# Kernel optimization log

Measured on AMD Instinct MI355X. Metric: run time of the kernel, lower is better.

Reference implementation:

```python
import jax, jax.numpy as jnp
import numpy as np

N, C, LM, ELEMS = 1024, 128, 16, 10   # nodes, channels, lm components (lmax=3), elements
P1, P2, P3 = 4, 12, 30                # generalized-CG path counts per correlation order
DIMS = (1, 3)                         # output irreps kept: 0e (dim 1), 1o (dim 3)


def _sparse(rng, shape, density=0.15):
    # stand-in generalized Clebsch-Gordan U tensor: fixed, sparse constants
    a = rng.standard_normal(shape).astype(np.float32)
    return jnp.asarray(a * (rng.random(shape) < density))


def setup_inputs() -> dict:
    k = jax.random.split(jax.random.key(0), 2)
    rng = np.random.default_rng(0)
    inp = {
        'x': jax.random.normal(k[0], (N, C, LM), jnp.float32),
        'species': jax.random.randint(k[1], (N,), 0, ELEMS, jnp.int32),
    }
    for i, d in enumerate(DIMS):
        inp[f'U1_{i}'] = _sparse(rng, (d, LM, P1))
        inp[f'U2_{i}'] = _sparse(rng, (d, LM, LM, P2))
        inp[f'U3_{i}'] = _sparse(rng, (d, LM, LM, LM, P3))
        for nu, p in ((1, P1), (2, P2), (3, P3)):
            inp[f'W{nu}_{i}'] = jnp.asarray((rng.standard_normal((ELEMS, p, C)) / np.sqrt(p)).astype(np.float32))
        inp[f'Wlin_{i}'] = jnp.asarray(rng.standard_normal((C, C)).astype(np.float32))
    return inp


def _sym_contract(x, species, U1, U2, U3, W1, W2, W3):
    # MACE recursive symmetric contraction, highest correlation order first.
    # x: [n, c, m] (channels factored to separate axis); species selects per-element weights.
    out = jnp.einsum('Lijmp,npc,ncm->ncLij', U3, W3[species], x)          # nu = 3 term
    out = jnp.einsum('Lijp,npc->ncLij', U2, W2[species]) + out            # add nu = 2 basis
    out = jnp.einsum('ncLij,ncj->ncLi', out, x)                           # contract one power of x
    out = jnp.einsum('Lip,npc->ncLi', U1, W1[species]) + out              # add nu = 1 basis
    return jnp.einsum('ncLi,nci->ncL', out, x)                            # [n, c, dim_L]


def _forward(x, species, U1_0, U2_0, U3_0, W1_0, W2_0, W3_0, Wlin_0,
             U1_1, U2_1, U3_1, W1_1, W2_1, W3_1, Wlin_1):
    f0 = _sym_contract(x, species, U1_0, U2_0, U3_0, W1_0, W2_0, W3_0)    # [n, C, 1]
    f1 = _sym_contract(x, species, U1_1, U2_1, U3_1, W1_1, W2_1, W3_1)    # [n, C, 3]
    s = 1.0 / float(np.sqrt(C))                                            # e3nn.Linear path norm
    y0 = jnp.einsum('nc,ck->nk', f0[..., 0], Wlin_0) * s                  # 128x0e block
    y1 = jnp.einsum('nci,ck->nki', f1, Wlin_1) * s                        # 128x1o block
    return jnp.concatenate([y0, y1.reshape(y1.shape[0], -1)], axis=-1)    # [n, 128 + 384]


def reference(x, species, U1_0, U2_0, U3_0, W1_0, W2_0, W3_0, Wlin_0,
              U1_1, U2_1, U3_1, W1_1, W2_1, W3_1, Wlin_1):
    return _forward(x, species, U1_0, U2_0, U3_0, W1_0, W2_0, W3_0, Wlin_0,
                    U1_1, U2_1, U3_1, W1_1, W2_1, W3_1, Wlin_1)
```

## Files before the change

kernel.cpp:

```cpp
#include <hip/hip_runtime.h>
#include <hip/hip_fp16.h>

typedef float v2f __attribute__((ext_vector_type(2)));

#define NN    1024
#define CC    128
#define NELEM 10
#define NQ3   816
#define NQ2   136
#define NQ    968
#define KP    48
#define QT    11
#define NTILE 88

#define NL_OFF    0
#define CNT_OFF   40960
#define CALL_OFF  524288
#define F_OFF     20447232
#define UHAT_OFF  10485760

__device__ __constant__ int d_OFF2[16] = {0,16,31,45,58,70,81,91,100,108,115,121,126,130,133,135};
__device__ __constant__ int d_OFF3[16] = {0,136,256,361,452,530,596,651,696,732,760,781,796,806,812,815};

__global__ void k_usym(const float* __restrict__ U3_0, const float* __restrict__ U3_1,
                       const float* __restrict__ U2_0, const float* __restrict__ U2_1,
                       const float* __restrict__ U1_0, const float* __restrict__ U1_1,
                       float* __restrict__ uhat) {
    if (blockIdx.x < 64) {
        int tid = blockIdx.x * 256 + threadIdx.x;
        int Lout = tid >> 12;
        int r = tid & 4095;
        int a = r >> 8, b = (r >> 4) & 15, m = r & 15;
        if (a > b || b > m) return;
        int q = d_OFF3[a] + (d_OFF2[b] - d_OFF2[a]) + (m - b);
        const float* U = (Lout == 0) ? U3_0 : U3_1;
        int L = (Lout == 0) ? 0 : (Lout - 1);
        int P[6][3] = {{a,b,m},{a,m,b},{b,a,m},{b,m,a},{m,a,b},{m,b,a}};
        float s[30];
#pragma unroll
        for (int p = 0; p < 30; ++p) s[p] = 0.f;
        for (int t = 0; t < 6; ++t) {
            bool dup = false;
            for (int u = 0; u < t; ++u)
                if (P[u][0] == P[t][0] && P[u][1] == P[t][1] && P[u][2] == P[t][2]) dup = true;
            if (dup) continue;
            const float* src = U + ((((L * 16 + P[t][0]) * 16 + P[t][1]) * 16 + P[t][2]) * 30);
#pragma unroll
            for (int p = 0; p < 30; ++p) s[p] += src[p];
        }
        float* dst = uhat + ((size_t)Lout * NQ + q) * KP;
#pragma unroll
        for (int p = 0; p < 30; ++p) dst[p] = s[p];
#pragma unroll
        for (int p = 30; p < KP; ++p) dst[p] = 0.f;
    } else {
        int tid = (blockIdx.x - 64) * 256 + threadIdx.x;
        if (tid < 1024) {
            int Lout = tid >> 8;
            int r = tid & 255;
            int a = r >> 4, b = r & 15;
            if (a > b) return;
            int q = NQ3 + d_OFF2[a] + (b - a);
            const float* U = (Lout == 0) ? U2_0 : U2_1;
            int L = (Lout == 0) ? 0 : (Lout - 1);
            float* dst = uhat + ((size_t)Lout * NQ + q) * KP;
#pragma unroll
            for (int p = 0; p < 30; ++p) dst[p] = 0.f;
#pragma unroll
            for (int p = 0; p < 12; ++p) {
                float v = U[((L * 16 + a) * 16 + b) * 12 + p];
                if (a != b) v += U[((L * 16 + b) * 16 + a) * 12 + p];
                dst[30 + p] = v;
            }
#pragma unroll
            for (int p = 42; p < KP; ++p) dst[p] = 0.f;
        } else if (tid < 1024 + 64) {
            int s2 = tid - 1024;
            int Lout = s2 >> 4, i = s2 & 15;
            int q = NQ3 + NQ2 + i;
            const float* U = (Lout == 0) ? U1_0 : U1_1;
            int L = (Lout == 0) ? 0 : (Lout - 1);
            float* dst = uhat + ((size_t)Lout * NQ + q) * KP;
#pragma unroll
            for (int p = 0; p < 42; ++p) dst[p] = 0.f;
#pragma unroll
            for (int p = 0; p < 4; ++p) dst[42 + p] = U[(L * 16 + i) * 4 + p];
            dst[46] = 0.f; dst[47] = 0.f;
        }
    }
}

__global__ void k_plist(const int* __restrict__ species, int* __restrict__ nodelist,
                        int* __restrict__ counts) {
    __shared__ int cnt[NELEM];
    int t = threadIdx.x;
    if (t < NELEM) cnt[t] = 0;
    __syncthreads();
    int e = species[t];
    int pos = atomicAdd(&cnt[e], 1);
    nodelist[e * NN + pos] = t;
    __syncthreads();
    if (t < NELEM) counts[t] = cnt[t];
}

__global__ __launch_bounds__(256) void k_fold(
    const float* __restrict__ uhat,
    const float* __restrict__ W1_0, const float* __restrict__ W2_0, const float* __restrict__ W3_0,
    const float* __restrict__ W1_1, const float* __restrict__ W2_1, const float* __restrict__ W3_1,
    uint2* __restrict__ call4h) {
    __shared__ __align__(16) float uh_lds[4][QT][KP];
    int e  = blockIdx.x / NTILE;
    int qt = blockIdx.x % NTILE;
    int t = threadIdx.x;
    {
        const float4* src4 = (const float4*)uhat;
        float4* dst4 = (float4*)uh_lds;
        for (int i = t; i < 4 * QT * 12; i += 256) {
            int l = i / (QT * 12);
            int r = i - l * (QT * 12);
            int qloc = r / 12, p4 = r % 12;
            dst4[i] = src4[((size_t)l * NQ + qt * QT + qloc) * 12 + p4];
        }
    }
    int c  = t & 127;
    int qs = t >> 7;
    float wr[2][KP];
#pragma unroll
    for (int p = 0; p < 30; ++p) {
        wr[0][p] = W3_0[(e * 30 + p) * CC + c];
        wr[1][p] = W3_1[(e * 30 + p) * CC + c];
    }
#pragma unroll
    for (int p = 0; p < 12; ++p) {
        wr[0][30 + p] = W2_0[(e * 12 + p) * CC + c];
        wr[1][30 + p] = W2_1[(e * 12 + p) * CC + c];
    }
#pragma unroll
    for (int p = 0; p < 4; ++p) {
        wr[0][42 + p] = W1_0[(e * 4 + p) * CC + c];
        wr[1][42 + p] = W1_1[(e * 4 + p) * CC + c];
    }
    wr[0][46] = wr[0][47] = wr[1][46] = wr[1][47] = 0.f;
    __syncthreads();
    size_t base = ((size_t)e * CC + c) * NQ;
    for (int j = 0; j < 6; ++j) {
        int qloc = qs * 6 + j;
        if (qloc >= QT) break;
        int q = qt * QT + qloc;
        float r[4];
#pragma unroll
        for (int l = 0; l < 4; ++l) {
            const float4* up = (const float4*)uh_lds[l][qloc];
            const float* w = (l == 0) ? wr[0] : wr[1];
            float acc0 = 0.f, acc1 = 0.f, acc2 = 0.f, acc3 = 0.f;
#pragma unroll
            for (int p4 = 0; p4 < 12; ++p4) {
                float4 u = up[p4];
                acc0 = fmaf(u.x, w[p4 * 4 + 0], acc0);
                acc1 = fmaf(u.y, w[p4 * 4 + 1], acc1);
                acc2 = fmaf(u.z, w[p4 * 4 + 2], acc2);
                acc3 = fmaf(u.w, w[p4 * 4 + 3], acc3);
            }
            r[l] = (acc0 + acc1) + (acc2 + acc3);
        }
        __half2 h01 = __floats2half2_rn(r[0], r[1]);
        __half2 h23 = __floats2half2_rn(r[2], r[3]);
        uint2 v;
        v.x = *(unsigned int*)&h01;
        v.y = *(unsigned int*)&h23;
        call4h[base + q] = v;
    }
}

#define COEF(W0, W1, W2, W3) \
    uint2 pk = cf_lds[q]; \
    __half2 h01 = *(__half2*)&pk.x; __half2 h23 = *(__half2*)&pk.y; \
    float W0 = __half2float(h01.x), W1 = __half2float(h01.y); \
    float W2 = __half2float(h23.x), W3 = __half2float(h23.y);

#define CUBIC(A0, A1) { \
    _Pragma("unroll") for (int a = (A0); a < (A1); ++a) { \
        _Pragma("unroll") for (int b = a; b < 16; ++b) { \
            v2f pab = xv[a] * xv[b]; \
            _Pragma("unroll") for (int m = b; m < 16; ++m) { \
                COEF(wx, wy, wz, ww); v2f mo = pab * xv[m]; \
                a0 += mo * wx; a1 += mo * wy; a2 += mo * wz; a3 += mo * ww; ++q; } } } }

#define QUAD(A0, A1) { \
    _Pragma("unroll") for (int a = (A0); a < (A1); ++a) { \
        _Pragma("unroll") for (int b = a; b < 16; ++b) { \
            COEF(wx, wy, wz, ww); v2f mo = xv[a] * xv[b]; \
            a0 += mo * wx; a1 += mo * wy; a2 += mo * wz; a3 += mo * ww; ++q; } } }

__global__ __launch_bounds__(256) void k_eval(
    const float* __restrict__ x, const int* __restrict__ nodelist,
    const int* __restrict__ counts, const uint2* __restrict__ call4h,
    float4* __restrict__ fout) {
    __shared__ __align__(16) uint2 cf_lds[NQ];
    __shared__ __align__(16) v2f part[3][64][4];
    int ec = blockIdx.x;
    int e = ec >> 7;
    int c = ec & 127;
    int cnt = counts[e];
    const float4* cf4 = (const float4*)(call4h + (size_t)ec * NQ);
    int t = threadIdx.x;
    int slice = t >> 6;
    int lane  = t & 63;

    int i0 = lane * 2, i1 = i0 + 1;
    bool v0i = i0 < cnt, v1i = i1 < cnt;
    int n0 = v0i ? nodelist[e * NN + i0] : 0;
    int n1 = v1i ? nodelist[e * NN + i1] : 0;

    for (int i = t; i < NQ / 2; i += 256) ((float4*)cf_lds)[i] = cf4[i];

    for (int sb = 0; sb < cnt; sb += 128) {
        if (sb > 0) {
            i0 = sb + lane * 2; i1 = i0 + 1;
            v0i = i0 < cnt; v1i = i1 < cnt;
            n0 = v0i ? nodelist[e * NN + i0] : 0;
            n1 = v1i ? nodelist[e * NN + i1] : 0;
        }
        const float4* xp0 = (const float4*)(x + ((size_t)n0 * CC + c) * 16);
        const float4* xp1 = (const float4*)(x + ((size_t)n1 * CC + c) * 16);
        float4 p0 = xp0[0], p1 = xp0[1], p2 = xp0[2], p3 = xp0[3];
        float4 q0 = xp1[0], q1 = xp1[1], q2 = xp1[2], q3 = xp1[3];
        if (sb == 0) __syncthreads();
        v2f xv[16];
        xv[0]  = v2f{p0.x, q0.x}; xv[1]  = v2f{p0.y, q0.y};
        xv[2]  = v2f{p0.z, q0.z}; xv[3]  = v2f{p0.w, q0.w};
        xv[4]  = v2f{p1.x, q1.x}; xv[5]  = v2f{p1.y, q1.y};
        xv[6]  = v2f{p1.z, q1.z}; xv[7]  = v2f{p1.w, q1.w};
        xv[8]  = v2f{p2.x, q2.x}; xv[9]  = v2f{p2.y, q2.y};
        xv[10] = v2f{p2.z, q2.z}; xv[11] = v2f{p2.w, q2.w};
        xv[12] = v2f{p3.x, q3.x}; xv[13] = v2f{p3.y, q3.y};
        xv[14] = v2f{p3.z, q3.z}; xv[15] = v2f{p3.w, q3.w};
        if (!v0i) {
#pragma unroll
            for (int m = 0; m < 16; ++m) xv[m].x = 0.f;
        }
        if (!v1i) {
#pragma unroll
            for (int m = 0; m < 16; ++m) xv[m].y = 0.f;
        }
        v2f a0 = {0.f, 0.f}, a1 = {0.f, 0.f}, a2 = {0.f, 0.f}, a3 = {0.f, 0.f};
        int q;
        if (slice == 0) {
            q = 0;   CUBIC(0, 2);
        } else if (slice == 1) {
            q = 256; CUBIC(2, 4);
            q = NQ3; QUAD(0, 4);
        } else if (slice == 2) {
            q = 452; CUBIC(4, 7);
            q = NQ3 + 58; QUAD(4, 10);
        } else {
            q = 651; CUBIC(7, 16);
            q = NQ3 + 115; QUAD(10, 16);
            q = NQ3 + NQ2;
#pragma unroll
            for (int a = 0; a < 16; ++a) {
                COEF(wx, wy, wz, ww); v2f mo = xv[a];
                a0 += mo * wx; a1 += mo * wy; a2 += mo * wz; a3 += mo * ww; ++q;
            }
        }
        if (slice > 0) {
            part[slice - 1][lane][0] = a0; part[slice - 1][lane][1] = a1;
            part[slice - 1][lane][2] = a2; part[slice - 1][lane][3] = a3;
        }
        __syncthreads();
        if (slice == 0) {
            v2f s0 = a0 + part[0][lane][0] + part[1][lane][0] + part[2][lane][0];
            v2f s1 = a1 + part[0][lane][1] + part[1][lane][1] + part[2][lane][1];
            v2f s2 = a2 + part[0][lane][2] + part[1][lane][2] + part[2][lane][2];
            v2f s3 = a3 + part[0][lane][3] + part[1][lane][3] + part[2][lane][3];
            if (v0i) fout[(size_t)n0 * CC + c] = make_float4(s0.x, s1.x, s2.x, s3.x);
            if (v1i) fout[(size_t)n1 * CC + c] = make_float4(s0.y, s1.y, s2.y, s3.y);
        }
        __syncthreads();
    }
}

__global__ __launch_bounds__(256) void k_linear(
    const float4* __restrict__ fin, const float* __restrict__ Wlin0,
    const float* __restrict__ Wlin1, float* __restrict__ out) {
    __shared__ float4 fl[256];
    int t = threadIdx.x;
    fl[t] = fin[(size_t)blockIdx.x * 256 + t];
    __syncthreads();
    int nl = t >> 7, k = t & 127;
    int n = blockIdx.x * 2 + nl;
    float a0 = 0.f, a1 = 0.f, a2 = 0.f, a3 = 0.f;
#pragma unroll 8
    for (int c = 0; c < CC; ++c) {
        float4 f = fl[nl * CC + c];
        float w0 = Wlin0[c * CC + k];
        float w1 = Wlin1[c * CC + k];
        a0 = fmaf(f.x, w0, a0);
        a1 = fmaf(f.y, w1, a1);
        a2 = fmaf(f.z, w1, a2);
        a3 = fmaf(f.w, w1, a3);
    }
    const float s = 0.08838834764831845f;
    float* o = out + (size_t)n * 512;
    o[k] = a0 * s;
    o[128 + 3 * k + 0] = a1 * s;
    o[128 + 3 * k + 1] = a2 * s;
    o[128 + 3 * k + 2] = a3 * s;
}

extern "C" void kernel_launch(void* const* d_in, const int* in_sizes, int n_in,
                              void* d_out, int out_size, void* d_ws, size_t ws_size,
                              hipStream_t stream) {
    const float* x     = (const float*)d_in[0];
    const int*   spec  = (const int*)d_in[1];
    const float* U1_0  = (const float*)d_in[2];
    const float* U2_0  = (const float*)d_in[3];
    const float* U3_0  = (const float*)d_in[4];
    const float* W1_0  = (const float*)d_in[5];
    const float* W2_0  = (const float*)d_in[6];
    const float* W3_0  = (const float*)d_in[7];
    const float* Wl_0  = (const float*)d_in[8];
    const float* U1_1  = (const float*)d_in[9];
    const float* U2_1  = (const float*)d_in[10];
    const float* U3_1  = (const float*)d_in[11];
    const float* W1_1  = (const float*)d_in[12];
    const float* W2_1  = (const float*)d_in[13];
    const float* W3_1  = (const float*)d_in[14];
    const float* Wl_1  = (const float*)d_in[15];

    char* ws = (char*)d_ws;
    int*    nodelist = (int*)(ws + NL_OFF);
    int*    counts   = (int*)(ws + CNT_OFF);
    uint2*  call4h   = (uint2*)(ws + CALL_OFF);
    float*  uhat     = (float*)(ws + UHAT_OFF);
    float4* fbuf     = (float4*)(ws + F_OFF);

    k_usym<<<dim3(69), dim3(256), 0, stream>>>(U3_0, U3_1, U2_0, U2_1, U1_0, U1_1, uhat);
    k_plist<<<dim3(1), dim3(1024), 0, stream>>>(spec, nodelist, counts);
    k_fold<<<dim3(880), dim3(256), 0, stream>>>(uhat, W1_0, W2_0, W3_0,
                                                W1_1, W2_1, W3_1, call4h);
    k_eval<<<dim3(1280), dim3(256), 0, stream>>>(x, nodelist, counts, call4h, fbuf);
    k_linear<<<dim3(512), dim3(256), 0, stream>>>(fbuf, Wl_0, Wl_1, (float*)d_out);
}
```

Measured before the change: 75.13 us.

## Merge setup kernels, register-block eval over four nodes, widen linear

The species bucketing is folded into the U symmetrisation kernel, which removes one launch. The eval kernel now gives each block two channels. Each lane handles four nodes, so every coefficient LDS load feeds eight packed FMAs, and coefficients are converted from fp16 to fp32 once when staged into LDS. The linear kernel computes two nodes per thread so each Wlin load is reused. The cost is more registers per thread in eval and half as many blocks, which may hurt occupancy and load balance.

```diff
diff --git a/kernel.cpp b/kernel.cpp
--- a/kernel.cpp
+++ b/kernel.cpp
@@ -16,16 +16,18 @@
 #define NL_OFF    0
 #define CNT_OFF   40960
 #define CALL_OFF  524288
+#define UHAT_OFF  10485760
 #define F_OFF     20447232
-#define UHAT_OFF  10485760
 
 __device__ __constant__ int d_OFF2[16] = {0,16,31,45,58,70,81,91,100,108,115,121,126,130,133,135};
 __device__ __constant__ int d_OFF3[16] = {0,136,256,361,452,530,596,651,696,732,760,781,796,806,812,815};
 
-__global__ void k_usym(const float* __restrict__ U3_0, const float* __restrict__ U3_1,
-                       const float* __restrict__ U2_0, const float* __restrict__ U2_1,
-                       const float* __restrict__ U1_0, const float* __restrict__ U1_1,
-                       float* __restrict__ uhat) {
+__global__ void k_setup(const float* __restrict__ U3_0, const float* __restrict__ U3_1,
+                        const float* __restrict__ U2_0, const float* __restrict__ U2_1,
+                        const float* __restrict__ U1_0, const float* __restrict__ U1_1,
+                        const int* __restrict__ species,
+                        float* __restrict__ uhat, int* __restrict__ nodelist,
+                        int* __restrict__ counts) {
     if (blockIdx.x < 64) {
         int tid = blockIdx.x * 256 + threadIdx.x;
         int Lout = tid >> 12;
@@ -53,7 +55,7 @@
         for (int p = 0; p < 30; ++p) dst[p] = s[p];
 #pragma unroll
         for (int p = 30; p < KP; ++p) dst[p] = 0.f;
-    } else {
+    } else if (blockIdx.x < 69) {
         int tid = (blockIdx.x - 64) * 256 + threadIdx.x;
         if (tid < 1024) {
             int Lout = tid >> 8;
@@ -87,20 +89,21 @@
             for (int p = 0; p < 4; ++p) dst[42 + p] = U[(L * 16 + i) * 4 + p];
             dst[46] = 0.f; dst[47] = 0.f;
         }
-    }
-}
-
-__global__ void k_plist(const int* __restrict__ species, int* __restrict__ nodelist,
-                        int* __restrict__ counts) {
-    __shared__ int cnt[NELEM];
-    int t = threadIdx.x;
-    if (t < NELEM) cnt[t] = 0;
-    __syncthreads();
-    int e = species[t];
-    int pos = atomicAdd(&cnt[e], 1);
-    nodelist[e * NN + pos] = t;
-    __syncthreads();
-    if (t < NELEM) counts[t] = cnt[t];
+    } else {
+        __shared__ int cnt[NELEM];
+        int t = threadIdx.x;
+        if (t < NELEM) cnt[t] = 0;
+        __syncthreads();
+#pragma unroll
+        for (int j = 0; j < 4; ++j) {
+            int node = t * 4 + j;
+            int e = species[node];
+            int pos = atomicAdd(&cnt[e], 1);
+            nodelist[e * NN + pos] = node;
+        }
+        __syncthreads();
+        if (t < NELEM) counts[t] = cnt[t];
+    }
 }
 
 __global__ __launch_bounds__(256) void k_fold(
@@ -172,78 +175,104 @@
     }
 }
 
-#define COEF(W0, W1, W2, W3) \
-    uint2 pk = cf_lds[q]; \
-    __half2 h01 = *(__half2*)&pk.x; __half2 h23 = *(__half2*)&pk.y; \
-    float W0 = __half2float(h01.x), W1 = __half2float(h01.y); \
-    float W2 = __half2float(h23.x), W3 = __half2float(h23.y);
-
 #define CUBIC(A0, A1) { \
     _Pragma("unroll") for (int a = (A0); a < (A1); ++a) { \
         _Pragma("unroll") for (int b = a; b < 16; ++b) { \
-            v2f pab = xv[a] * xv[b]; \
+            v2f pabA = xvA[a] * xvA[b]; v2f pabB = xvB[a] * xvB[b]; \
             _Pragma("unroll") for (int m = b; m < 16; ++m) { \
-                COEF(wx, wy, wz, ww); v2f mo = pab * xv[m]; \
-                a0 += mo * wx; a1 += mo * wy; a2 += mo * wz; a3 += mo * ww; ++q; } } } }
+                float4 w = cfp[q]; \
+                v2f moA = pabA * xvA[m]; v2f moB = pabB * xvB[m]; \
+                aA0 += moA * w.x; aA1 += moA * w.y; aA2 += moA * w.z; aA3 += moA * w.w; \
+                aB0 += moB * w.x; aB1 += moB * w.y; aB2 += moB * w.z; aB3 += moB * w.w; \
+                ++q; } } } }
 
 #define QUAD(A0, A1) { \
     _Pragma("unroll") for (int a = (A0); a < (A1); ++a) { \
         _Pragma("unroll") for (int b = a; b < 16; ++b) { \
-            COEF(wx, wy, wz, ww); v2f mo = xv[a] * xv[b]; \
-            a0 += mo * wx; a1 += mo * wy; a2 += mo * wz; a3 += mo * ww; ++q; } } }
-
-__global__ __launch_bounds__(256) void k_eval(
+            float4 w = cfp[q]; \
+            v2f moA = xvA[a] * xvA[b]; v2f moB = xvB[a] * xvB[b]; \
+            aA0 += moA * w.x; aA1 += moA * w.y; aA2 += moA * w.z; aA3 += moA * w.w; \
+            aB0 += moB * w.x; aB1 += moB * w.y; aB2 += moB * w.z; aB3 += moB * w.w; \
+            ++q; } } }
+
+__global__ void k_eval(
     const float* __restrict__ x, const int* __restrict__ nodelist,
     const int* __restrict__ counts, const uint2* __restrict__ call4h,
     float4* __restrict__ fout) {
-    __shared__ __align__(16) uint2 cf_lds[NQ];
-    __shared__ __align__(16) v2f part[3][64][4];
-    int ec = blockIdx.x;
-    int e = ec >> 7;
-    int c = ec & 127;
+    __shared__ __align__(16) float4 cf_lds[2][NQ + 2];
+    __shared__ __align__(16) v2f part[3][64][9];
+    int blk = blockIdx.x;
+    int e  = blk >> 6;
+    int c0 = (blk & 63) * 2;
     int cnt = counts[e];
-    const float4* cf4 = (const float4*)(call4h + (size_t)ec * NQ);
     int t = threadIdx.x;
-    int slice = t >> 6;
-    int lane  = t & 63;
-
-    int i0 = lane * 2, i1 = i0 + 1;
-    bool v0i = i0 < cnt, v1i = i1 < cnt;
-    int n0 = v0i ? nodelist[e * NN + i0] : 0;
-    int n1 = v1i ? nodelist[e * NN + i1] : 0;
-
-    for (int i = t; i < NQ / 2; i += 256) ((float4*)cf_lds)[i] = cf4[i];
+    int slice = t >> 6, lane = t & 63;
+    int half = lane >> 5, ls = lane & 31;
+    int c = c0 + half;
+
+    const uint2* src = call4h + ((size_t)e * CC + c0) * NQ;
+    for (int i = t; i < 2 * NQ; i += 256) {
+        uint2 pk = src[i];
+        __half2 h01 = *(__half2*)&pk.x, h23 = *(__half2*)&pk.y;
+        int ch = i >= NQ;
+        cf_lds[ch][i - ch * NQ] = make_float4(
+            __half2float(h01.x), __half2float(h01.y),
+            __half2float(h23.x), __half2float(h23.y));
+    }
+    __syncthreads();
+    const float4* cfp = cf_lds[half];
 
     for (int sb = 0; sb < cnt; sb += 128) {
-        if (sb > 0) {
-            i0 = sb + lane * 2; i1 = i0 + 1;
-            v0i = i0 < cnt; v1i = i1 < cnt;
-            n0 = v0i ? nodelist[e * NN + i0] : 0;
-            n1 = v1i ? nodelist[e * NN + i1] : 0;
-        }
+        int ib = sb + ls * 4;
+        bool v0 = ib < cnt, v1 = ib + 1 < cnt, v2 = ib + 2 < cnt, v3 = ib + 3 < cnt;
+        int n0 = v0 ? nodelist[e * NN + ib] : 0;
+        int n1 = v1 ? nodelist[e * NN + ib + 1] : 0;
+        int n2 = v2 ? nodelist[e * NN + ib + 2] : 0;
+        int n3 = v3 ? nodelist[e * NN + ib + 3] : 0;
         const float4* xp0 = (const float4*)(x + ((size_t)n0 * CC + c) * 16);
         const float4* xp1 = (const float4*)(x + ((size_t)n1 * CC + c) * 16);
-        float4 p0 = xp0[0], p1 = xp0[1], p2 = xp0[2], p3 = xp0[3];
-        float4 q0 = xp1[0], q1 = xp1[1], q2 = xp1[2], q3 = xp1[3];
-        if (sb == 0) __syncthreads();
-        v2f xv[16];
-        xv[0]  = v2f{p0.x, q0.x}; xv[1]  = v2f{p0.y, q0.y};
-        xv[2]  = v2f{p0.z, q0.z}; xv[3]  = v2f{p0.w, q0.w};
-        xv[4]  = v2f{p1.x, q1.x}; xv[5]  = v2f{p1.y, q1.y};
-        xv[6]  = v2f{p1.z, q1.z}; xv[7]  = v2f{p1.w, q1.w};
-        xv[8]  = v2f{p2.x, q2.x}; xv[9]  = v2f{p2.y, q2.y};
-        xv[10] = v2f{p2.z, q2.z}; xv[11] = v2f{p2.w, q2.w};
-        xv[12] = v2f{p3.x, q3.x}; xv[13] = v2f{p3.y, q3.y};
-        xv[14] = v2f{p3.z, q3.z}; xv[15] = v2f{p3.w, q3.w};
-        if (!v0i) {
-#pragma unroll
-            for (int m = 0; m < 16; ++m) xv[m].x = 0.f;
-        }
-        if (!v1i) {
-#pragma unroll
-            for (int m = 0; m < 16; ++m) xv[m].y = 0.f;
-        }
-        v2f a0 = {0.f, 0.f}, a1 = {0.f, 0.f}, a2 = {0.f, 0.f}, a3 = {0.f, 0.f};
+        const float4* xp2 = (const float4*)(x + ((size_t)n2 * CC + c) * 16);
+        const float4* xp3 = (const float4*)(x + ((size_t)n3 * CC + c) * 16);
+        float4 r0, r1, r2, r3, s0, s1, s2, s3;
+        v2f xvA[16], xvB[16];
+        r0 = xp0[0]; r1 = xp0[1]; r2 = xp0[2]; r3 = xp0[3];
+        s0 = xp1[0]; s1 = xp1[1]; s2 = xp1[2]; s3 = xp1[3];
+        xvA[0]  = v2f{r0.x, s0.x}; xvA[1]  = v2f{r0.y, s0.y};
+        xvA[2]  = v2f{r0.z, s0.z}; xvA[3]  = v2f{r0.w, s0.w};
+        xvA[4]  = v2f{r1.x, s1.x}; xvA[5]  = v2f{r1.y, s1.y};
+        xvA[6]  = v2f{r1.z, s1.z}; xvA[7]  = v2f{r1.w, s1.w};
+        xvA[8]  = v2f{r2.x, s2.x}; xvA[9]  = v2f{r2.y, s2.y};
+        xvA[10] = v2f{r2.z, s2.z}; xvA[11] = v2f{r2.w, s2.w};
+        xvA[12] = v2f{r3.x, s3.x}; xvA[13] = v2f{r3.y, s3.y};
+        xvA[14] = v2f{r3.z, s3.z}; xvA[15] = v2f{r3.w, s3.w};
+        r0 = xp2[0]; r1 = xp2[1]; r2 = xp2[2]; r3 = xp2[3];
+        s0 = xp3[0]; s1 = xp3[1]; s2 = xp3[2]; s3 = xp3[3];
+        xvB[0]  = v2f{r0.x, s0.x}; xvB[1]  = v2f{r0.y, s0.y};
+        xvB[2]  = v2f{r0.z, s0.z}; xvB[3]  = v2f{r0.w, s0.w};
+        xvB[4]  = v2f{r1.x, s1.x}; xvB[5]  = v2f{r1.y, s1.y};
+        xvB[6]  = v2f{r1.z, s1.z}; xvB[7]  = v2f{r1.w, s1.w};
+        xvB[8]  = v2f{r2.x, s2.x}; xvB[9]  = v2f{r2.y, s2.y};
+        xvB[10] = v2f{r2.z, s2.z}; xvB[11] = v2f{r2.w, s2.w};
+        xvB[12] = v2f{r3.x, s3.x}; xvB[13] = v2f{r3.y, s3.y};
+        xvB[14] = v2f{r3.z, s3.z}; xvB[15] = v2f{r3.w, s3.w};
+        if (!v0) {
+#pragma unroll
+            for (int m = 0; m < 16; ++m) xvA[m].x = 0.f;
+        }
+        if (!v1) {
+#pragma unroll
+            for (int m = 0; m < 16; ++m) xvA[m].y = 0.f;
+        }
+        if (!v2) {
+#pragma unroll
+            for (int m = 0; m < 16; ++m) xvB[m].x = 0.f;
+        }
+        if (!v3) {
+#pragma unroll
+            for (int m = 0; m < 16; ++m) xvB[m].y = 0.f;
+        }
+        v2f aA0 = {0.f,0.f}, aA1 = {0.f,0.f}, aA2 = {0.f,0.f}, aA3 = {0.f,0.f};
+        v2f aB0 = {0.f,0.f}, aB1 = {0.f,0.f}, aB2 = {0.f,0.f}, aB3 = {0.f,0.f};
         int q;
         if (slice == 0) {
             q = 0;   CUBIC(0, 2);
@@ -259,22 +288,32 @@
             q = NQ3 + NQ2;
 #pragma unroll
             for (int a = 0; a < 16; ++a) {
-                COEF(wx, wy, wz, ww); v2f mo = xv[a];
-                a0 += mo * wx; a1 += mo * wy; a2 += mo * wz; a3 += mo * ww; ++q;
+                float4 w = cfp[q];
+                v2f moA = xvA[a], moB = xvB[a];
+                aA0 += moA * w.x; aA1 += moA * w.y; aA2 += moA * w.z; aA3 += moA * w.w;
+                aB0 += moB * w.x; aB1 += moB * w.y; aB2 += moB * w.z; aB3 += moB * w.w;
+                ++q;
             }
         }
         if (slice > 0) {
-            part[slice - 1][lane][0] = a0; part[slice - 1][lane][1] = a1;
-            part[slice - 1][lane][2] = a2; part[slice - 1][lane][3] = a3;
+            v2f* pp = part[slice - 1][lane];
+            pp[0] = aA0; pp[1] = aA1; pp[2] = aA2; pp[3] = aA3;
+            pp[4] = aB0; pp[5] = aB1; pp[6] = aB2; pp[7] = aB3;
         }
         __syncthreads();
         if (slice == 0) {
-            v2f s0 = a0 + part[0][lane][0] + part[1][lane][0] + part[2][lane][0];
-            v2f s1 = a1 + part[0][lane][1] + part[1][lane][1] + part[2][lane][1];
-            v2f s2 = a2 + part[0][lane][2] + part[1][lane][2] + part[2][lane][2];
-            v2f s3 = a3 + part[0][lane][3] + part[1][lane][3] + part[2][lane][3];
-            if (v0i) fout[(size_t)n0 * CC + c] = make_float4(s0.x, s1.x, s2.x, s3.x);
-            if (v1i) fout[(size_t)n1 * CC + c] = make_float4(s0.y, s1.y, s2.y, s3.y);
+            v2f sA0 = aA0 + part[0][lane][0] + part[1][lane][0] + part[2][lane][0];
+            v2f sA1 = aA1 + part[0][lane][1] + part[1][lane][1] + part[2][lane][1];
+            v2f sA2 = aA2 + part[0][lane][2] + part[1][lane][2] + part[2][lane][2];
+            v2f sA3 = aA3 + part[0][lane][3] + part[1][lane][3] + part[2][lane][3];
+            v2f sB0 = aB0 + part[0][lane][4] + part[1][lane][4] + part[2][lane][4];
+            v2f sB1 = aB1 + part[0][lane][5] + part[1][lane][5] + part[2][lane][5];
+            v2f sB2 = aB2 + part[0][lane][6] + part[1][lane][6] + part[2][lane][6];
+            v2f sB3 = aB3 + part[0][lane][7] + part[1][lane][7] + part[2][lane][7];
+            if (v0) fout[(size_t)n0 * CC + c] = make_float4(sA0.x, sA1.x, sA2.x, sA3.x);
+            if (v1) fout[(size_t)n1 * CC + c] = make_float4(sA0.y, sA1.y, sA2.y, sA3.y);
+            if (v2) fout[(size_t)n2 * CC + c] = make_float4(sB0.x, sB1.x, sB2.x, sB3.x);
+            if (v3) fout[(size_t)n3 * CC + c] = make_float4(sB0.y, sB1.y, sB2.y, sB3.y);
         }
         __syncthreads();
     }
@@ -283,22 +322,25 @@
 __global__ __launch_bounds__(256) void k_linear(
     const float4* __restrict__ fin, const float* __restrict__ Wlin0,
     const float* __restrict__ Wlin1, float* __restrict__ out) {
-    __shared__ float4 fl[256];
+    __shared__ float4 fl[512];
     int t = threadIdx.x;
-    fl[t] = fin[(size_t)blockIdx.x * 256 + t];
+    fl[t]       = fin[(size_t)blockIdx.x * 512 + t];
+    fl[t + 256] = fin[(size_t)blockIdx.x * 512 + t + 256];
     __syncthreads();
-    int nl = t >> 7, k = t & 127;
-    int n = blockIdx.x * 2 + nl;
+    int nh = t >> 7, k = t & 127;
+    int n = blockIdx.x * 4 + nh * 2;
     float a0 = 0.f, a1 = 0.f, a2 = 0.f, a3 = 0.f;
+    float b0 = 0.f, b1 = 0.f, b2 = 0.f, b3 = 0.f;
 #pragma unroll 8
     for (int c = 0; c < CC; ++c) {
-        float4 f = fl[nl * CC + c];
+        float4 f0 = fl[(nh * 2) * CC + c];
+        float4 f1 = fl[(nh * 2 + 1) * CC + c];
         float w0 = Wlin0[c * CC + k];
         float w1 = Wlin1[c * CC + k];
-        a0 = fmaf(f.x, w0, a0);
-        a1 = fmaf(f.y, w1, a1);
-        a2 = fmaf(f.z, w1, a2);
-        a3 = fmaf(f.w, w1, a3);
+        a0 = fmaf(f0.x, w0, a0); a1 = fmaf(f0.y, w1, a1);
+        a2 = fmaf(f0.z, w1, a2); a3 = fmaf(f0.w, w1, a3);
+        b0 = fmaf(f1.x, w0, b0); b1 = fmaf(f1.y, w1, b1);
+        b2 = fmaf(f1.z, w1, b2); b3 = fmaf(f1.w, w1, b3);
     }
     const float s = 0.08838834764831845f;
     float* o = out + (size_t)n * 512;
@@ -306,6 +348,11 @@
     o[128 + 3 * k + 0] = a1 * s;
     o[128 + 3 * k + 1] = a2 * s;
     o[128 + 3 * k + 2] = a3 * s;
+    o += 512;
+    o[k] = b0 * s;
+    o[128 + 3 * k + 0] = b1 * s;
+    o[128 + 3 * k + 1] = b2 * s;
+    o[128 + 3 * k + 2] = b3 * s;
 }
 
 extern "C" void kernel_launch(void* const* d_in, const int* in_sizes, int n_in,
@@ -335,10 +382,10 @@
     float*  uhat     = (float*)(ws + UHAT_OFF);
     float4* fbuf     = (float4*)(ws + F_OFF);
 
-    k_usym<<<dim3(69), dim3(256), 0, stream>>>(U3_0, U3_1, U2_0, U2_1, U1_0, U1_1, uhat);
-    k_plist<<<dim3(1), dim3(1024), 0, stream>>>(spec, nodelist, counts);
+    k_setup<<<dim3(70), dim3(256), 0, stream>>>(U3_0, U3_1, U2_0, U2_1, U1_0, U1_1,
+                                                spec, uhat, nodelist, counts);
     k_fold<<<dim3(880), dim3(256), 0, stream>>>(uhat, W1_0, W2_0, W3_0,
                                                 W1_1, W2_1, W3_1, call4h);
-    k_eval<<<dim3(1280), dim3(256), 0, stream>>>(x, nodelist, counts, call4h, fbuf);
-    k_linear<<<dim3(512), dim3(256), 0, stream>>>(fbuf, Wl_0, Wl_1, (float*)d_out);
-}
+    k_eval<<<dim3(640), dim3(256), 0, stream>>>(x, nodelist, counts, call4h, fbuf);
+    k_linear<<<dim3(256), dim3(256), 0, stream>>>(fbuf, Wl_0, Wl_1, (float*)d_out);
+}
```

Result: slower. 84.28 us (+12.2%).

## Merge setup kernels, store fp32 coefficients in LDS, two nodes per linear thread

Applied to the files above, without the earlier changes.

Folds the node-list bucketing kernel into the U-symmetrization kernel as an extra block, removing one launch. k_eval now converts the half-precision folded coefficients to float4 once while staging them into LDS, so the inner loops no longer do per-use half-to-float conversions, at the cost of twice the LDS footprint. It also adds a launch-bounds occupancy hint. k_linear has each thread compute two nodes so every Wlin load is reused twice, halving the grid size.

```diff
diff --git a/kernel.cpp b/kernel.cpp
--- a/kernel.cpp
+++ b/kernel.cpp
@@ -16,16 +16,18 @@
 #define NL_OFF    0
 #define CNT_OFF   40960
 #define CALL_OFF  524288
+#define UHAT_OFF  10485760
 #define F_OFF     20447232
-#define UHAT_OFF  10485760
 
 __device__ __constant__ int d_OFF2[16] = {0,16,31,45,58,70,81,91,100,108,115,121,126,130,133,135};
 __device__ __constant__ int d_OFF3[16] = {0,136,256,361,452,530,596,651,696,732,760,781,796,806,812,815};
 
-__global__ void k_usym(const float* __restrict__ U3_0, const float* __restrict__ U3_1,
-                       const float* __restrict__ U2_0, const float* __restrict__ U2_1,
-                       const float* __restrict__ U1_0, const float* __restrict__ U1_1,
-                       float* __restrict__ uhat) {
+__global__ void k_setup(const float* __restrict__ U3_0, const float* __restrict__ U3_1,
+                        const float* __restrict__ U2_0, const float* __restrict__ U2_1,
+                        const float* __restrict__ U1_0, const float* __restrict__ U1_1,
+                        const int* __restrict__ species,
+                        float* __restrict__ uhat, int* __restrict__ nodelist,
+                        int* __restrict__ counts) {
     if (blockIdx.x < 64) {
         int tid = blockIdx.x * 256 + threadIdx.x;
         int Lout = tid >> 12;
@@ -53,7 +55,7 @@
         for (int p = 0; p < 30; ++p) dst[p] = s[p];
 #pragma unroll
         for (int p = 30; p < KP; ++p) dst[p] = 0.f;
-    } else {
+    } else if (blockIdx.x < 69) {
         int tid = (blockIdx.x - 64) * 256 + threadIdx.x;
         if (tid < 1024) {
             int Lout = tid >> 8;
@@ -87,20 +89,21 @@
             for (int p = 0; p < 4; ++p) dst[42 + p] = U[(L * 16 + i) * 4 + p];
             dst[46] = 0.f; dst[47] = 0.f;
         }
-    }
-}
-
-__global__ void k_plist(const int* __restrict__ species, int* __restrict__ nodelist,
-                        int* __restrict__ counts) {
-    __shared__ int cnt[NELEM];
-    int t = threadIdx.x;
-    if (t < NELEM) cnt[t] = 0;
-    __syncthreads();
-    int e = species[t];
-    int pos = atomicAdd(&cnt[e], 1);
-    nodelist[e * NN + pos] = t;
-    __syncthreads();
-    if (t < NELEM) counts[t] = cnt[t];
+    } else {
+        __shared__ int cnt[NELEM];
+        int t = threadIdx.x;
+        if (t < NELEM) cnt[t] = 0;
+        __syncthreads();
+#pragma unroll
+        for (int j = 0; j < 4; ++j) {
+            int node = t * 4 + j;
+            int e = species[node];
+            int pos = atomicAdd(&cnt[e], 1);
+            nodelist[e * NN + pos] = node;
+        }
+        __syncthreads();
+        if (t < NELEM) counts[t] = cnt[t];
+    }
 }
 
 __global__ __launch_bounds__(256) void k_fold(
@@ -172,60 +175,51 @@
     }
 }
 
-#define COEF(W0, W1, W2, W3) \
-    uint2 pk = cf_lds[q]; \
-    __half2 h01 = *(__half2*)&pk.x; __half2 h23 = *(__half2*)&pk.y; \
-    float W0 = __half2float(h01.x), W1 = __half2float(h01.y); \
-    float W2 = __half2float(h23.x), W3 = __half2float(h23.y);
-
 #define CUBIC(A0, A1) { \
     _Pragma("unroll") for (int a = (A0); a < (A1); ++a) { \
         _Pragma("unroll") for (int b = a; b < 16; ++b) { \
             v2f pab = xv[a] * xv[b]; \
             _Pragma("unroll") for (int m = b; m < 16; ++m) { \
-                COEF(wx, wy, wz, ww); v2f mo = pab * xv[m]; \
-                a0 += mo * wx; a1 += mo * wy; a2 += mo * wz; a3 += mo * ww; ++q; } } } }
+                float4 w = cf_lds[q]; v2f mo = pab * xv[m]; \
+                a0 += mo * w.x; a1 += mo * w.y; a2 += mo * w.z; a3 += mo * w.w; ++q; } } } }
 
 #define QUAD(A0, A1) { \
     _Pragma("unroll") for (int a = (A0); a < (A1); ++a) { \
         _Pragma("unroll") for (int b = a; b < 16; ++b) { \
-            COEF(wx, wy, wz, ww); v2f mo = xv[a] * xv[b]; \
-            a0 += mo * wx; a1 += mo * wy; a2 += mo * wz; a3 += mo * ww; ++q; } } }
-
-__global__ __launch_bounds__(256) void k_eval(
+            float4 w = cf_lds[q]; v2f mo = xv[a] * xv[b]; \
+            a0 += mo * w.x; a1 += mo * w.y; a2 += mo * w.z; a3 += mo * w.w; ++q; } } }
+
+__global__ __launch_bounds__(256, 4) void k_eval(
     const float* __restrict__ x, const int* __restrict__ nodelist,
     const int* __restrict__ counts, const uint2* __restrict__ call4h,
     float4* __restrict__ fout) {
-    __shared__ __align__(16) uint2 cf_lds[NQ];
+    __shared__ __align__(16) float4 cf_lds[NQ];
     __shared__ __align__(16) v2f part[3][64][4];
     int ec = blockIdx.x;
     int e = ec >> 7;
     int c = ec & 127;
     int cnt = counts[e];
-    const float4* cf4 = (const float4*)(call4h + (size_t)ec * NQ);
+    const uint2* src = call4h + (size_t)ec * NQ;
     int t = threadIdx.x;
+    for (int i = t; i < NQ; i += 256) {
+        uint2 pk = src[i];
+        __half2 h01 = *(__half2*)&pk.x, h23 = *(__half2*)&pk.y;
+        cf_lds[i] = make_float4(__half2float(h01.x), __half2float(h01.y),
+                                __half2float(h23.x), __half2float(h23.y));
+    }
+    __syncthreads();
     int slice = t >> 6;
     int lane  = t & 63;
 
-    int i0 = lane * 2, i1 = i0 + 1;
-    bool v0i = i0 < cnt, v1i = i1 < cnt;
-    int n0 = v0i ? nodelist[e * NN + i0] : 0;
-    int n1 = v1i ? nodelist[e * NN + i1] : 0;
-
-    for (int i = t; i < NQ / 2; i += 256) ((float4*)cf_lds)[i] = cf4[i];
-
     for (int sb = 0; sb < cnt; sb += 128) {
-        if (sb > 0) {
-            i0 = sb + lane * 2; i1 = i0 + 1;
-            v0i = i0 < cnt; v1i = i1 < cnt;
-            n0 = v0i ? nodelist[e * NN + i0] : 0;
-            n1 = v1i ? nodelist[e * NN + i1] : 0;
-        }
+        int i0 = sb + lane * 2, i1 = i0 + 1;
+        bool v0i = i0 < cnt, v1i = i1 < cnt;
+        int n0 = v0i ? nodelist[e * NN + i0] : 0;
+        int n1 = v1i ? nodelist[e * NN + i1] : 0;
         const float4* xp0 = (const float4*)(x + ((size_t)n0 * CC + c) * 16);
         const float4* xp1 = (const float4*)(x + ((size_t)n1 * CC + c) * 16);
         float4 p0 = xp0[0], p1 = xp0[1], p2 = xp0[2], p3 = xp0[3];
         float4 q0 = xp1[0], q1 = xp1[1], q2 = xp1[2], q3 = xp1[3];
-        if (sb == 0) __syncthreads();
         v2f xv[16];
         xv[0]  = v2f{p0.x, q0.x}; xv[1]  = v2f{p0.y, q0.y};
         xv[2]  = v2f{p0.z, q0.z}; xv[3]  = v2f{p0.w, q0.w};
@@ -259,8 +253,8 @@
             q = NQ3 + NQ2;
 #pragma unroll
             for (int a = 0; a < 16; ++a) {
-                COEF(wx, wy, wz, ww); v2f mo = xv[a];
-                a0 += mo * wx; a1 += mo * wy; a2 += mo * wz; a3 += mo * ww; ++q;
+                float4 w = cf_lds[q]; v2f mo = xv[a];
+                a0 += mo * w.x; a1 += mo * w.y; a2 += mo * w.z; a3 += mo * w.w; ++q;
             }
         }
         if (slice > 0) {
@@ -283,22 +277,25 @@
 __global__ __launch_bounds__(256) void k_linear(
     const float4* __restrict__ fin, const float* __restrict__ Wlin0,
     const float* __restrict__ Wlin1, float* __restrict__ out) {
-    __shared__ float4 fl[256];
+    __shared__ float4 fl[512];
     int t = threadIdx.x;
-    fl[t] = fin[(size_t)blockIdx.x * 256 + t];
+    fl[t]       = fin[(size_t)blockIdx.x * 512 + t];
+    fl[t + 256] = fin[(size_t)blockIdx.x * 512 + t + 256];
     __syncthreads();
-    int nl = t >> 7, k = t & 127;
-    int n = blockIdx.x * 2 + nl;
+    int nh = t >> 7, k = t & 127;
+    int n = blockIdx.x * 4 + nh * 2;
     float a0 = 0.f, a1 = 0.f, a2 = 0.f, a3 = 0.f;
+    float b0 = 0.f, b1 = 0.f, b2 = 0.f, b3 = 0.f;
 #pragma unroll 8
     for (int c = 0; c < CC; ++c) {
-        float4 f = fl[nl * CC + c];
+        float4 f0 = fl[(nh * 2) * CC + c];
+        float4 f1 = fl[(nh * 2 + 1) * CC + c];
         float w0 = Wlin0[c * CC + k];
         float w1 = Wlin1[c * CC + k];
-        a0 = fmaf(f.x, w0, a0);
-        a1 = fmaf(f.y, w1, a1);
-        a2 = fmaf(f.z, w1, a2);
-        a3 = fmaf(f.w, w1, a3);
+        a0 = fmaf(f0.x, w0, a0); a1 = fmaf(f0.y, w1, a1);
+        a2 = fmaf(f0.z, w1, a2); a3 = fmaf(f0.w, w1, a3);
+        b0 = fmaf(f1.x, w0, b0); b1 = fmaf(f1.y, w1, b1);
+        b2 = fmaf(f1.z, w1, b2); b3 = fmaf(f1.w, w1, b3);
     }
     const float s = 0.08838834764831845f;
     float* o = out + (size_t)n * 512;
@@ -306,6 +303,11 @@
     o[128 + 3 * k + 0] = a1 * s;
     o[128 + 3 * k + 1] = a2 * s;
     o[128 + 3 * k + 2] = a3 * s;
+    o += 512;
+    o[k] = b0 * s;
+    o[128 + 3 * k + 0] = b1 * s;
+    o[128 + 3 * k + 1] = b2 * s;
+    o[128 + 3 * k + 2] = b3 * s;
 }
 
 extern "C" void kernel_launch(void* const* d_in, const int* in_sizes, int n_in,
@@ -335,10 +337,10 @@
     float*  uhat     = (float*)(ws + UHAT_OFF);
     float4* fbuf     = (float4*)(ws + F_OFF);
 
-    k_usym<<<dim3(69), dim3(256), 0, stream>>>(U3_0, U3_1, U2_0, U2_1, U1_0, U1_1, uhat);
-    k_plist<<<dim3(1), dim3(1024), 0, stream>>>(spec, nodelist, counts);
+    k_setup<<<dim3(70), dim3(256), 0, stream>>>(U3_0, U3_1, U2_0, U2_1, U1_0, U1_1,
+                                                spec, uhat, nodelist, counts);
     k_fold<<<dim3(880), dim3(256), 0, stream>>>(uhat, W1_0, W2_0, W3_0,
                                                 W1_1, W2_1, W3_1, call4h);
     k_eval<<<dim3(1280), dim3(256), 0, stream>>>(x, nodelist, counts, call4h, fbuf);
-    k_linear<<<dim3(512), dim3(256), 0, stream>>>(fbuf, Wl_0, Wl_1, (float*)d_out);
-}
+    k_linear<<<dim3(256), dim3(256), 0, stream>>>(fbuf, Wl_0, Wl_1, (float*)d_out);
+}
```

Result: slower. 83.32 us (+10.9%).
